# Performance work log

Hardware: AMD Instinct MI355X
Metric: run time of the kernel (lower is better)

Reference implementation:

```python
import jax, jax.numpy as jnp
import numpy as np

NUM_TRAIN = 256  # num_train_anchors
N, A, T = 8, 131072, 64


def _make_boxes(key, shape2):
    # shape2 = (..., 2) of (y, x); returns valid boxes (y1, x1, y2, x2) in [0, 1]
    k1, k2 = jax.random.split(key)
    c1 = jax.random.uniform(k1, shape2, dtype=jnp.float32)
    c2 = jax.random.uniform(k2, shape2, dtype=jnp.float32)
    lo = jnp.minimum(c1, c2)
    hi = jnp.maximum(c1, c2)
    return jnp.stack([lo[..., 0], lo[..., 1], hi[..., 0], hi[..., 1]], axis=-1)


def setup_inputs() -> dict:
    key = jax.random.key(0)
    ka, kt, kp, kn = jax.random.split(key, 4)
    return {
        "anchors": _make_boxes(ka, (N, A, 2)),
        "true_bboxes": _make_boxes(kt, (N, T, 2)),
        "rand_pos": jax.random.uniform(kp, (N, A), dtype=jnp.float32),
        "rand_neg": jax.random.uniform(kn, (N, A), dtype=jnp.float32),
    }


def _bbox_overlap(anchors, gt):
    # anchors [A,4], gt [T,4] -> IoU [A,T]
    ay1, ax1, ay2, ax2 = [anchors[:, i] for i in range(4)]
    gy1, gx1, gy2, gx2 = [gt[:, i] for i in range(4)]
    a_area = (ay2 - ay1) * (ax2 - ax1)                       # [A]
    g_area = (gy2 - gy1) * (gx2 - gx1)                       # [T]
    ih = jnp.clip(jnp.minimum(ay2[:, None], gy2[None, :]) - jnp.maximum(ay1[:, None], gy1[None, :]), 0.0)
    iw = jnp.clip(jnp.minimum(ax2[:, None], gx2[None, :]) - jnp.maximum(ax1[:, None], gx1[None, :]), 0.0)
    inter = ih * iw                                          # [A,T]
    union = a_area[:, None] + g_area[None, :] - inter
    return jnp.where(union > 0, inter / jnp.where(union > 0, union, 1.0), 0.0)


def _rank_of(scores):
    # rank[i] = position of element i in ascending sort of scores
    order = jnp.argsort(scores)
    return jnp.zeros(scores.shape[0], jnp.int32).at[order].set(jnp.arange(scores.shape[0], dtype=jnp.int32))


def _compute_bbox_deltas(anchors, gt):
    # standard (dy, dx, dh, dw) encoding with safe denominators
    ah = anchors[:, 2] - anchors[:, 0]
    aw = anchors[:, 3] - anchors[:, 1]
    acy = anchors[:, 0] + 0.5 * ah
    acx = anchors[:, 1] + 0.5 * aw
    gh = gt[:, 2] - gt[:, 0]
    gw = gt[:, 3] - gt[:, 1]
    gcy = gt[:, 0] + 0.5 * gh
    gcx = gt[:, 1] + 0.5 * gw
    ah_s = jnp.where(ah > 0, ah, 1.0)
    aw_s = jnp.where(aw > 0, aw, 1.0)
    gh_s = jnp.where(gh > 0, gh, 1.0)
    gw_s = jnp.where(gw > 0, gw, 1.0)
    return jnp.stack([(gcy - acy) / ah_s, (gcx - acx) / aw_s,
                      jnp.log(gh_s / ah_s), jnp.log(gw_s / aw_s)], axis=-1)


def _get_targets(anchors, gt, r_pos, r_neg):
    na = anchors.shape[0]
    # strip_out_of_bounds_anchors: zero out anchors falling outside [0,1]^2 (keeps static shape)
    inb = (anchors[:, 0] >= 0) & (anchors[:, 1] >= 0) & (anchors[:, 2] <= 1) & (anchors[:, 3] <= 1)
    anchors = jnp.where(inb[:, None], anchors, 0.0)

    overlaps = _bbox_overlap(anchors, gt)                    # [A,T]

    # --- class assignment ---
    iou_max_val = jnp.max(overlaps, axis=1)                  # [A]
    classes = jnp.full((na,), -1, jnp.int32)
    classes = jnp.where(iou_max_val < 0.3, 0, classes)
    iou_max_anchor = jnp.argmax(overlaps, axis=0)            # [T] best anchor per gt
    pos_anchor = jnp.zeros((na,), jnp.int32).at[iou_max_anchor].set(1)
    classes = jnp.where(pos_anchor > 0, 1, classes)
    classes = jnp.where(iou_max_val >= 0.7, 1, classes)

    # --- subsample positives to NUM_TRAIN//2 (uniform random subset) ---
    pos = classes > 0
    rank_p = _rank_of(jnp.where(pos, r_pos, jnp.inf))
    keep_pos = pos & (rank_p < NUM_TRAIN // 2)
    classes = jnp.where(pos & ~keep_pos, -1, classes)
    n_pos = jnp.sum(keep_pos.astype(jnp.int32))

    # --- subsample negatives to NUM_TRAIN - n_pos ---
    desired_neg = NUM_TRAIN - n_pos
    neg = classes == 0
    rank_n = _rank_of(jnp.where(neg, r_neg, jnp.inf))
    keep_neg = neg & (rank_n < desired_neg)
    classes = jnp.where(neg & ~keep_neg, -1, classes)

    # --- deltas for positive anchors ---
    best_gt = jnp.argmax(overlaps, axis=1)                   # [A]
    deltas = _compute_bbox_deltas(anchors, gt[best_gt])      # [A,4]
    deltas = jnp.where((classes > 0)[:, None], deltas, 0.0)
    return classes, deltas


def reference(anchors, true_bboxes, rand_pos, rand_neg):
    classes, deltas = jax.vmap(_get_targets)(anchors, true_bboxes, rand_pos, rand_neg)
    return classes, deltas
```

## Files before the change

kernel.cpp:

```cpp
#include <hip/hip_runtime.h>
#include <stdint.h>

#define N_B 8
#define A_N 131072
#define T_N 64
#define NUM_TRAIN 256
#define NEG_TAU 0.05f
#define ITEM_CAP 512
#define HSET 512
#define APT 2
#define SEG_A 512
#define GBLK_A 256
#define CAPP 128
#define BLK_C 128
#define SEG_C 1024

typedef unsigned long long u64;
typedef unsigned int u32;

__device__ __forceinline__ u64 aload64(const u64* p) {
    return __hip_atomic_load((u64*)p, __ATOMIC_RELAXED, __HIP_MEMORY_SCOPE_AGENT);
}
__device__ __forceinline__ int aload32(const int* p) {
    return __hip_atomic_load((int*)p, __ATOMIC_RELAXED, __HIP_MEMORY_SCOPE_AGENT);
}
__device__ __forceinline__ void astore64(u64* p, u64 v) {
    __hip_atomic_store(p, v, __ATOMIC_RELAXED, __HIP_MEMORY_SCOPE_AGENT);
}
__device__ __forceinline__ void astore32(int* p, int v) {
    __hip_atomic_store(p, v, __ATOMIC_RELAXED, __HIP_MEMORY_SCOPE_AGENT);
}

__device__ __forceinline__ float iou_one(float ay1, float ax1, float ay2, float ax2,
                                         float a_area, float gy1, float gx1, float gy2,
                                         float gx2, float g_area) {
#pragma clang fp contract(off)
    float ih = fmaxf(fminf(ay2, gy2) - fmaxf(ay1, gy1), 0.0f);
    float iw = fmaxf(fminf(ax2, gx2) - fmaxf(ax1, gx1), 0.0f);
    float inter = ih * iw;
    float uni = (a_area + g_area) - inter;
    return uni > 0.0f ? inter / uni : 0.0f;
}

__device__ __forceinline__ bool in_hset(const int* hset, int a) {
    u32 h = ((u32)a * 2654435761u) >> 23 & (HSET - 1);
    while (true) {
        int v = hset[h];
        if (v == -1) return false;
        if (v == a) return true;
        h = (h + 1) & (HSET - 1);
    }
}

__device__ u64 tail_select(const u64* list, const int* cnts,
                           const u64* extras, int ecnt, const int* hset, bool use_excl,
                           int k, float scale, u64 ovf_all,
                           int* hist, u64* items, int* misc, int* wsum, u64* result) {
    int tid = threadIdx.x, lane = tid & 63, wid = tid >> 6;
    if (tid == 0) { misc[0] = 0; *result = ovf_all; }
    __syncthreads();

    int h = hist[tid], v = h;
#pragma unroll
    for (int d = 1; d < 64; d <<= 1) {
        int t = __shfl_up(v, d, 64);
        if (lane >= d) v += t;
    }
    if (lane == 63) wsum[wid] = v;
    __syncthreads();
    int total = wsum[0] + wsum[1] + wsum[2] + wsum[3];
    int base = 0;
    for (int w = 0; w < wid; w++) base += wsum[w];
    int incl = base + v, exc = incl - h;
    if (k >= exc && k < incl) { misc[1] = tid; misc[2] = exc; }
    if (tid == 0) misc[3] = total;
    __syncthreads();
    if (k >= total) return ovf_all;
    int b = misc[1], before = misc[2];

#define PROC(P) do { u64 p_ = (P); int a_ = (int)(u32)p_;                                   \
        if (!use_excl || !in_hset(hset, a_)) {                                              \
            float v_ = __uint_as_float((u32)(p_ >> 32));                                    \
            int bn_ = (int)(v_ * scale); bn_ = bn_ > 255 ? 255 : bn_;                       \
            if (bn_ == b) { int ix_ = atomicAdd(&misc[0], 1);                               \
                            if (ix_ < ITEM_CAP) items[ix_] = p_; } } } while (0)

    int c = aload32(&cnts[tid]);
    const u64* lp = list + ((size_t)tid << 7);
    for (int ci = 0; ci < c; ci += 4) {
        u64 p0 = aload64(&lp[ci]);
        u64 p1 = (ci + 1 < c) ? aload64(&lp[ci + 1]) : 0;
        u64 p2 = (ci + 2 < c) ? aload64(&lp[ci + 2]) : 0;
        u64 p3 = (ci + 3 < c) ? aload64(&lp[ci + 3]) : 0;
        PROC(p0);
        if (ci + 1 < c) PROC(p1);
        if (ci + 2 < c) PROC(p2);
        if (ci + 3 < c) PROC(p3);
    }
    for (int i = tid; i < ecnt; i += 256) PROC(extras[i]);
#undef PROC
    __syncthreads();
    int m = misc[0]; m = m < ITEM_CAP ? m : ITEM_CAP;
    int target = k - before;
    for (int i = tid; i < m; i += 256) {
        u64 p = items[i];
        int r = 0;
        for (int j = 0; j < m; j++) r += (items[j] < p);
        if (r == target) *result = p;
    }
    __syncthreads();
    u64 res = *result;
    __syncthreads();
    return res;
}

__global__ void __launch_bounds__(256) k_main(const float4* __restrict__ anchors4,
                                              const float4* __restrict__ gts4,
                                              const float* __restrict__ rpos,
                                              const float* __restrict__ rneg,
                                              unsigned char* __restrict__ preclass,
                                              long long* __restrict__ colpack,
                                              u64* __restrict__ pos_list,
                                              u64* __restrict__ neg_list,
                                              int* __restrict__ bcp, int* __restrict__ bcn,
                                              int* __restrict__ hist_pos,
                                              int* __restrict__ hist_neg,
                                              int* __restrict__ done_cnt,
                                              u64* __restrict__ cutoff) {
    __shared__ float4 gbox[T_N];
    __shared__ float gars[T_N];
    __shared__ u64 cmax[T_N];
    __shared__ int lcnt[2];
    __shared__ signed char c0s[SEG_A];
    __shared__ int hist[256];
    __shared__ u64 items[ITEM_CAP];
    __shared__ int hset[HSET];
    __shared__ u64 extras[T_N];
    __shared__ int wnrs[T_N];
    __shared__ int misc[4];
    __shared__ int wsum[4];
    __shared__ int shr[4];
    __shared__ u64 result;
    __shared__ int slast;

    int n = blockIdx.y, bx = blockIdx.x, tid = threadIdx.x, lane = tid & 63;
    int a0 = bx * SEG_A + tid;
    size_t nA = (size_t)n * A_N;

    if (tid < T_N) {
        float4 gb = gts4[n * T_N + tid];
        gbox[tid] = gb;
        {
#pragma clang fp contract(off)
            gars[tid] = (gb.z - gb.x) * (gb.w - gb.y);
        }
        cmax[tid] = 0;
    }
    if (tid < 2) lcnt[tid] = 0;
    __syncthreads();

    float ay1[APT], ax1[APT], ay2[APT], ax2[APT], aar[APT], vmax[APT];
#pragma unroll
    for (int k = 0; k < APT; k++) {
        float4 ab = anchors4[nA + a0 + k * 256];
        float y1 = ab.x, x1 = ab.y, y2 = ab.z, x2 = ab.w;
        bool inb = (y1 >= 0.f) && (x1 >= 0.f) && (y2 <= 1.f) && (x2 <= 1.f);
        if (!inb) { y1 = x1 = y2 = x2 = 0.f; }
        ay1[k] = y1; ax1[k] = x1; ay2[k] = y2; ax2[k] = x2;
        {
#pragma clang fp contract(off)
            aar[k] = (y2 - y1) * (x2 - x1);
        }
        vmax[k] = 0.f;
    }

#pragma unroll 4
    for (int jj = 0; jj < T_N; jj++) {
        int j = (lane + jj) & (T_N - 1);
        float4 gb = gbox[j];
        float gar = gars[j];
        float vb = iou_one(ay1[0], ax1[0], ay2[0], ax2[0], aar[0], gb.x, gb.y, gb.z, gb.w, gar);
        vmax[0] = fmaxf(vmax[0], vb);
        int kb = 0;
#pragma unroll
        for (int k = 1; k < APT; k++) {
            float v = iou_one(ay1[k], ax1[k], ay2[k], ax2[k], aar[k], gb.x, gb.y, gb.z, gb.w, gar);
            vmax[k] = fmaxf(vmax[k], v);
            if (v > vb) { vb = v; kb = k; }
        }
        u64 pk = ((u64)__float_as_uint(vb) << 32) | (u32)(~(u32)(a0 + (kb << 8)));
        atomicMax(&cmax[j], pk);
    }

    size_t segbase = ((size_t)(n * GBLK_A + bx)) << 7;
#pragma unroll
    for (int k = 0; k < APT; k++) {
        int a = a0 + k * 256;
        float vm = vmax[k];
        int c0 = (vm < 0.3f) ? 0 : ((vm >= 0.7f) ? 1 : -1);
        c0s[tid + k * 256] = (signed char)c0;
        preclass[nA + a] = (unsigned char)(signed char)c0;
        if (c0 == 1) {
            float rp = rpos[nA + a];
            int sl = atomicAdd(&lcnt[0], 1);
            if (sl < CAPP) {
                astore64(&pos_list[segbase + sl], ((u64)__float_as_uint(rp) << 32) | (u32)a);
                int bb = (int)(rp * 256.0f); bb = bb > 255 ? 255 : bb;
                atomicAdd(&hist_pos[(n << 8) + bb], 1);
            }
        } else if (c0 == 0) {
            float rn = rneg[nA + a];
            if (rn < NEG_TAU) {
                int sl = atomicAdd(&lcnt[1], 1);
                if (sl < CAPP) {
                    astore64(&neg_list[segbase + sl], ((u64)__float_as_uint(rn) << 32) | (u32)a);
                    int bb = (int)(rn * (256.0f / NEG_TAU)); bb = bb > 255 ? 255 : bb;
                    atomicAdd(&hist_neg[(n << 8) + bb], 1);
                }
            }
        }
    }
    __syncthreads();

    if (tid < T_N) {
        u64 m = cmax[tid];
        u32 wg = ~(u32)m;
        int wl = (int)wg - bx * SEG_A;
        u32 enc = (u32)c0s[wl] & 3u;
        u64 pk = (m & 0xFFFFFFFF00000000ull) | (u32)(~((wg << 2) | enc));
        atomicMax(&colpack[(n << 6) + tid], (long long)pk);
    }
    if (tid == 0) {
        astore32(&bcp[n * GBLK_A + bx], lcnt[0] < CAPP ? lcnt[0] : CAPP);
        astore32(&bcn[n * GBLK_A + bx], lcnt[1] < CAPP ? lcnt[1] : CAPP);
    }

    asm volatile("s_waitcnt vmcnt(0) lgkmcnt(0)" ::: "memory");
    __syncthreads();
    if (tid == 0) slast = (atomicAdd(&done_cnt[n], 1) == GBLK_A - 1) ? 1 : 0;
    __syncthreads();
    if (!slast) return;

    for (int i = tid; i < HSET; i += 256) hset[i] = -1;
    hist[tid] = aload32(&hist_pos[(n << 8) + tid]);
    __syncthreads();

    int w = 0, pcv = 0;
    bool dup = false;
    if (tid < T_N) {
        u64 m = aload64((const u64*)&colpack[(n << 6) + tid]);
        u32 ie = ~(u32)m;
        w = (int)(ie >> 2);
        pcv = ((ie & 3u) == 3u) ? -1 : (int)(ie & 3u);
        wnrs[tid] = w;
        u32 hh = ((u32)w * 2654435761u) >> 23 & (HSET - 1);
        while (true) {
            int old = atomicCAS(&hset[hh], -1, w);
            if (old == -1 || old == w) break;
            hh = (hh + 1) & (HSET - 1);
        }
    }
    __syncthreads();
    if (tid < T_N) {
        for (int t2 = 0; t2 < tid; t2++) dup |= (wnrs[t2] == w);
        bool val = !dup && (pcv != 1);
        u64 mask = __ballot(val);
        if (val) {
            int ix = (int)__popcll(mask & ((1ull << tid) - 1));
            extras[ix] = ((u64)__float_as_uint(rpos[nA + w]) << 32) | (u32)w;
        }
        if (tid == 0) shr[0] = (int)__popcll(mask);
    }
    __syncthreads();
    int extra_cnt = shr[0];
    for (int i = tid; i < extra_cnt; i += 256) {
        float vv = __uint_as_float((u32)(extras[i] >> 32));
        int bb = (int)(vv * 256.0f); bb = bb > 255 ? 255 : bb;
        atomicAdd(&hist[bb], 1);
    }
    __syncthreads();

    u64 cp = tail_select(pos_list + (((size_t)n * GBLK_A) << 7), bcp + n * GBLK_A,
                         extras, extra_cnt, hset, false,
                         NUM_TRAIN / 2, 256.0f, ~0ull,
                         hist, items, misc, wsum, &result);
    int P = misc[3];

    hist[tid] = aload32(&hist_neg[(n << 8) + tid]);
    __syncthreads();
    if (tid < T_N && !dup && pcv == 0) {
        float r = rneg[nA + w];
        if (r < NEG_TAU) {
            int bb = (int)(r * (256.0f / NEG_TAU)); bb = bb > 255 ? 255 : bb;
            atomicAdd(&hist[bb], -1);
        }
    }
    __syncthreads();
    int n_pos = P < NUM_TRAIN / 2 ? P : NUM_TRAIN / 2;
    u64 cn = tail_select(neg_list + (((size_t)n * GBLK_A) << 7), bcn + n * GBLK_A,
                         nullptr, 0, hset, true,
                         NUM_TRAIN - n_pos, 256.0f / NEG_TAU,
                         ((u64)__float_as_uint(NEG_TAU) << 32),
                         hist, items, misc, wsum, &result);
    if (tid == 0) {
        cutoff[2 * n] = cp;
        cutoff[2 * n + 1] = cn;
    }
}

__global__ void __launch_bounds__(256) k_C(const float4* __restrict__ anchors4,
                                           const float4* __restrict__ gts4,
                                           const u32* __restrict__ preclass32,
                                           const long long* __restrict__ colpack,
                                           const float4* __restrict__ rpos4,
                                           const float4* __restrict__ rneg4,
                                           const u64* __restrict__ cutoff,
                                           float4* __restrict__ out_classes4,
                                           float4* __restrict__ out_deltas) {
    __shared__ float4 gbox[T_N];
    __shared__ float gars[T_N];
    __shared__ u32 wbm[32];
    __shared__ u32 pbm[32];
    int n = blockIdx.y, bx = blockIdx.x, tid = threadIdx.x;
    size_t nA = (size_t)n * A_N;
    if (tid < 32) { wbm[tid] = 0; pbm[tid] = 0; }
    __syncthreads();
    if (tid < T_N) {
        float4 gb = gts4[n * T_N + tid];
        gbox[tid] = gb;
        {
#pragma clang fp contract(off)
            gars[tid] = (gb.z - gb.x) * (gb.w - gb.y);
        }
        int w = (int)((~(u32)(u64)colpack[(n << 6) + tid]) >> 2);
        int d = w - bx * SEG_C;
        if ((u32)d < (u32)SEG_C) atomicOr(&wbm[d >> 5], 1u << (d & 31));
    }
    __syncthreads();

    size_t gi4 = nA / 4 + bx * 256 + tid;
    u32 pcw = preclass32[gi4];
    float4 rp = rpos4[gi4];
    float4 rn = rneg4[gi4];
    float rpv[4] = {rp.x, rp.y, rp.z, rp.w};
    float rnv[4] = {rn.x, rn.y, rn.z, rn.w};
    int a0 = (bx * 256 + tid) * 4;
    u64 cp = cutoff[2 * n], cn = cutoff[2 * n + 1];

    u32 marked = (wbm[tid >> 3] >> ((tid & 7) * 4)) & 0xF;

    float fcv[4];
#pragma unroll
    for (int j = 0; j < 4; j++) {
        int c = (int)(signed char)((pcw >> (8 * j)) & 0xFF);
        if ((marked >> j) & 1) c = 1;
        int a = a0 + j;
        int fc = -1;
        if (c == 1) {
            u64 p = ((u64)__float_as_uint(rpv[j]) << 32) | (u32)a;
            fc = (p < cp) ? 1 : -1;
        } else if (c == 0) {
            u64 p = ((u64)__float_as_uint(rnv[j]) << 32) | (u32)a;
            fc = (p < cn) ? 0 : -1;
        }
        fcv[j] = (float)fc;
        if (fc == 1) {
            int s = 4 * tid + j;
            atomicOr(&pbm[s >> 5], 1u << (s & 31));
        }
    }
    out_classes4[gi4] = make_float4(fcv[0], fcv[1], fcv[2], fcv[3]);
    __syncthreads();

    int base = bx * SEG_C;
#pragma unroll
    for (int j = 0; j < 4; j++) {
        int s = j * 256 + tid;
        float4 d = make_float4(0.f, 0.f, 0.f, 0.f);
        if ((pbm[s >> 5] >> (s & 31)) & 1) {
            int a = base + s;
            float4 ab = anchors4[nA + a];
            float ay1 = ab.x, ax1 = ab.y, ay2 = ab.z, ax2 = ab.w;
            bool inb = (ay1 >= 0.f) && (ax1 >= 0.f) && (ay2 <= 1.f) && (ax2 <= 1.f);
            if (!inb) { ay1 = ax1 = ay2 = ax2 = 0.f; }
            float a_area;
            {
#pragma clang fp contract(off)
                a_area = (ay2 - ay1) * (ax2 - ax1);
            }
            float vm = 0.f; int jb = 0;
            for (int t = 0; t < T_N; t++) {
                float4 gb = gbox[t];
                float v = iou_one(ay1, ax1, ay2, ax2, a_area, gb.x, gb.y, gb.z, gb.w, gars[t]);
                bool g = v > vm;
                vm = g ? v : vm;
                jb = g ? t : jb;
            }
            float4 gb = gbox[jb];
            float ah = ay2 - ay1, aw = ax2 - ax1;
            float acy = ay1 + 0.5f * ah, acx = ax1 + 0.5f * aw;
            float gh = gb.z - gb.x, gw = gb.w - gb.y;
            float gcy = gb.x + 0.5f * gh, gcx = gb.y + 0.5f * gw;
            float ah_s = ah > 0.f ? ah : 1.f, aw_s = aw > 0.f ? aw : 1.f;
            float gh_s = gh > 0.f ? gh : 1.f, gw_s = gw > 0.f ? gw : 1.f;
            d.x = (gcy - acy) / ah_s;
            d.y = (gcx - acx) / aw_s;
            d.z = logf(gh_s / ah_s);
            d.w = logf(gw_s / aw_s);
        }
        out_deltas[nA + base + s] = d;
    }
}

extern "C" void kernel_launch(void* const* d_in, const int* in_sizes, int n_in,
                              void* d_out, int out_size, void* d_ws, size_t ws_size,
                              hipStream_t stream) {
    const float4* anchors4 = (const float4*)d_in[0];
    const float4* gts4     = (const float4*)d_in[1];
    const float*  rpos     = (const float*)d_in[2];
    const float*  rneg     = (const float*)d_in[3];

    char* p = (char*)d_ws;
    int* hist_pos_g = (int*)p; p += N_B * 256 * sizeof(int);
    int* hist_neg_g = (int*)p; p += N_B * 256 * sizeof(int);
    int* done_cnt   = (int*)p; p += N_B * sizeof(int);
    u64* cutoff   = (u64*)p;  p += 2 * N_B * sizeof(u64);
    long long* colpack = (long long*)p; p += N_B * T_N * sizeof(long long);
    u64* pos_list = (u64*)p;  p += (size_t)N_B * GBLK_A * CAPP * sizeof(u64);
    u64* neg_list = (u64*)p;  p += (size_t)N_B * GBLK_A * CAPP * sizeof(u64);
    unsigned char* preclass = (unsigned char*)p; p += (size_t)N_B * A_N;
    int* bcp  = (int*)p;  p += N_B * GBLK_A * sizeof(int);
    int* bcn  = (int*)p;  p += N_B * GBLK_A * sizeof(int);

    float4* out_classes4 = (float4*)d_out;
    float4* out_deltas   = (float4*)((float*)d_out + (size_t)N_B * A_N);

    hipMemsetAsync(hist_pos_g, 0, (2 * N_B * 256 + N_B) * sizeof(int), stream);

    k_main<<<dim3(GBLK_A, N_B), 256, 0, stream>>>(anchors4, gts4, rpos, rneg, preclass,
                                                  colpack, pos_list, neg_list, bcp, bcn,
                                                  hist_pos_g, hist_neg_g, done_cnt, cutoff);
    k_C<<<dim3(BLK_C, N_B), 256, 0, stream>>>(anchors4, gts4, (const u32*)preclass,
                                              colpack, (const float4*)rpos,
                                              (const float4*)rneg, cutoff,
                                              out_classes4, out_deltas);
}
```

Measured before the change: 184.7 us.

## Bucket candidate anchors by histogram bin instead of per-block lists

Candidate positive and negative anchors are now written into per-bin global buckets, with slots taken from the histogram atomic counter itself, instead of per-block lists. In the last block's tail selection, only the bucket of the selected bin is scanned rather than every block's list. This removes the per-block shared counters and count arrays and shrinks the serial scan each tail thread does. The cost is heavy global atomic contention on the histogram counters. Candidates are silently dropped if a bin overflows its cap, and the smaller item cap raises the same risk.

Measured after the change: 167.5 us, median of 2. 9.3% less time.

```diff
diff --git a/kernel.cpp b/kernel.cpp
--- a/kernel.cpp
+++ b/kernel.cpp
@@ -6,12 +6,12 @@
 #define T_N 64
 #define NUM_TRAIN 256
 #define NEG_TAU 0.05f
-#define ITEM_CAP 512
+#define ITEM_CAP 256
 #define HSET 512
 #define APT 2
 #define SEG_A 512
 #define GBLK_A 256
-#define CAPP 128
+#define BINCAP 128
 #define BLK_C 128
 #define SEG_C 1024
 
@@ -25,9 +25,6 @@
     return __hip_atomic_load((int*)p, __ATOMIC_RELAXED, __HIP_MEMORY_SCOPE_AGENT);
 }
 __device__ __forceinline__ void astore64(u64* p, u64 v) {
-    __hip_atomic_store(p, v, __ATOMIC_RELAXED, __HIP_MEMORY_SCOPE_AGENT);
-}
-__device__ __forceinline__ void astore32(int* p, int v) {
     __hip_atomic_store(p, v, __ATOMIC_RELAXED, __HIP_MEMORY_SCOPE_AGENT);
 }
 
@@ -52,7 +49,7 @@
     }
 }
 
-__device__ u64 tail_select(const u64* list, const int* cnts,
+__device__ u64 tail_select(const u64* bybin, const int* gcnt,
                            const u64* extras, int ecnt, const int* hset, bool use_excl,
                            int k, float scale, u64 ovf_all,
                            int* hist, u64* items, int* misc, int* wsum, u64* result) {
@@ -78,27 +75,21 @@
     if (k >= total) return ovf_all;
     int b = misc[1], before = misc[2];
 
-#define PROC(P) do { u64 p_ = (P); int a_ = (int)(u32)p_;                                   \
-        if (!use_excl || !in_hset(hset, a_)) {                                              \
-            float v_ = __uint_as_float((u32)(p_ >> 32));                                    \
-            int bn_ = (int)(v_ * scale); bn_ = bn_ > 255 ? 255 : bn_;                       \
-            if (bn_ == b) { int ix_ = atomicAdd(&misc[0], 1);                               \
-                            if (ix_ < ITEM_CAP) items[ix_] = p_; } } } while (0)
-
-    int c = aload32(&cnts[tid]);
-    const u64* lp = list + ((size_t)tid << 7);
-    for (int ci = 0; ci < c; ci += 4) {
-        u64 p0 = aload64(&lp[ci]);
-        u64 p1 = (ci + 1 < c) ? aload64(&lp[ci + 1]) : 0;
-        u64 p2 = (ci + 2 < c) ? aload64(&lp[ci + 2]) : 0;
-        u64 p3 = (ci + 3 < c) ? aload64(&lp[ci + 3]) : 0;
-        PROC(p0);
-        if (ci + 1 < c) PROC(p1);
-        if (ci + 2 < c) PROC(p2);
-        if (ci + 3 < c) PROC(p3);
-    }
-    for (int i = tid; i < ecnt; i += 256) PROC(extras[i]);
-#undef PROC
+    int stored = gcnt[b]; stored = stored > BINCAP ? BINCAP : stored;
+    for (int i = tid; i < stored; i += 256) {
+        u64 p = aload64(&bybin[(size_t)b * BINCAP + i]);
+        int a = (int)(u32)p;
+        if (!use_excl || !in_hset(hset, a)) {
+            int ix = atomicAdd(&misc[0], 1);
+            if (ix < ITEM_CAP) items[ix] = p;
+        }
+    }
+    for (int i = tid; i < ecnt; i += 256) {
+        u64 p = extras[i];
+        float vv = __uint_as_float((u32)(p >> 32));
+        int bn = (int)(vv * scale); bn = bn > 255 ? 255 : bn;
+        if (bn == b) { int ix = atomicAdd(&misc[0], 1); if (ix < ITEM_CAP) items[ix] = p; }
+    }
     __syncthreads();
     int m = misc[0]; m = m < ITEM_CAP ? m : ITEM_CAP;
     int target = k - before;
@@ -120,9 +111,8 @@
                                               const float* __restrict__ rneg,
                                               unsigned char* __restrict__ preclass,
                                               long long* __restrict__ colpack,
-                                              u64* __restrict__ pos_list,
-                                              u64* __restrict__ neg_list,
-                                              int* __restrict__ bcp, int* __restrict__ bcn,
+                                              u64* __restrict__ pos_bybin,
+                                              u64* __restrict__ neg_bybin,
                                               int* __restrict__ hist_pos,
                                               int* __restrict__ hist_neg,
                                               int* __restrict__ done_cnt,
@@ -130,9 +120,9 @@
     __shared__ float4 gbox[T_N];
     __shared__ float gars[T_N];
     __shared__ u64 cmax[T_N];
-    __shared__ int lcnt[2];
     __shared__ signed char c0s[SEG_A];
     __shared__ int hist[256];
+    __shared__ int gcnt[256];
     __shared__ u64 items[ITEM_CAP];
     __shared__ int hset[HSET];
     __shared__ u64 extras[T_N];
@@ -156,7 +146,6 @@
         }
         cmax[tid] = 0;
     }
-    if (tid < 2) lcnt[tid] = 0;
     __syncthreads();
 
     float ay1[APT], ax1[APT], ay2[APT], ax2[APT], aar[APT], vmax[APT];
@@ -192,7 +181,6 @@
         atomicMax(&cmax[j], pk);
     }
 
-    size_t segbase = ((size_t)(n * GBLK_A + bx)) << 7;
 #pragma unroll
     for (int k = 0; k < APT; k++) {
         int a = a0 + k * 256;
@@ -202,21 +190,19 @@
         preclass[nA + a] = (unsigned char)(signed char)c0;
         if (c0 == 1) {
             float rp = rpos[nA + a];
-            int sl = atomicAdd(&lcnt[0], 1);
-            if (sl < CAPP) {
-                astore64(&pos_list[segbase + sl], ((u64)__float_as_uint(rp) << 32) | (u32)a);
-                int bb = (int)(rp * 256.0f); bb = bb > 255 ? 255 : bb;
-                atomicAdd(&hist_pos[(n << 8) + bb], 1);
-            }
+            int bb = (int)(rp * 256.0f); bb = bb > 255 ? 255 : bb;
+            int sl = atomicAdd(&hist_pos[(n << 8) + bb], 1);
+            if (sl < BINCAP)
+                astore64(&pos_bybin[(size_t)((n << 8) + bb) * BINCAP + sl],
+                         ((u64)__float_as_uint(rp) << 32) | (u32)a);
         } else if (c0 == 0) {
             float rn = rneg[nA + a];
             if (rn < NEG_TAU) {
-                int sl = atomicAdd(&lcnt[1], 1);
-                if (sl < CAPP) {
-                    astore64(&neg_list[segbase + sl], ((u64)__float_as_uint(rn) << 32) | (u32)a);
-                    int bb = (int)(rn * (256.0f / NEG_TAU)); bb = bb > 255 ? 255 : bb;
-                    atomicAdd(&hist_neg[(n << 8) + bb], 1);
-                }
+                int bb = (int)(rn * (256.0f / NEG_TAU)); bb = bb > 255 ? 255 : bb;
+                int sl = atomicAdd(&hist_neg[(n << 8) + bb], 1);
+                if (sl < BINCAP)
+                    astore64(&neg_bybin[(size_t)((n << 8) + bb) * BINCAP + sl],
+                             ((u64)__float_as_uint(rn) << 32) | (u32)a);
             }
         }
     }
@@ -230,10 +216,6 @@
         u64 pk = (m & 0xFFFFFFFF00000000ull) | (u32)(~((wg << 2) | enc));
         atomicMax(&colpack[(n << 6) + tid], (long long)pk);
     }
-    if (tid == 0) {
-        astore32(&bcp[n * GBLK_A + bx], lcnt[0] < CAPP ? lcnt[0] : CAPP);
-        astore32(&bcn[n * GBLK_A + bx], lcnt[1] < CAPP ? lcnt[1] : CAPP);
-    }
 
     asm volatile("s_waitcnt vmcnt(0) lgkmcnt(0)" ::: "memory");
     __syncthreads();
@@ -242,7 +224,11 @@
     if (!slast) return;
 
     for (int i = tid; i < HSET; i += 256) hset[i] = -1;
-    hist[tid] = aload32(&hist_pos[(n << 8) + tid]);
+    {
+        int g = aload32(&hist_pos[(n << 8) + tid]);
+        gcnt[tid] = g;
+        hist[tid] = g;
+    }
     __syncthreads();
 
     int w = 0, pcv = 0;
@@ -280,13 +266,17 @@
     }
     __syncthreads();
 
-    u64 cp = tail_select(pos_list + (((size_t)n * GBLK_A) << 7), bcp + n * GBLK_A,
+    u64 cp = tail_select(pos_bybin + ((size_t)(n << 8)) * BINCAP, gcnt,
                          extras, extra_cnt, hset, false,
                          NUM_TRAIN / 2, 256.0f, ~0ull,
                          hist, items, misc, wsum, &result);
     int P = misc[3];
 
-    hist[tid] = aload32(&hist_neg[(n << 8) + tid]);
+    {
+        int g = aload32(&hist_neg[(n << 8) + tid]);
+        gcnt[tid] = g;
+        hist[tid] = g;
+    }
     __syncthreads();
     if (tid < T_N && !dup && pcv == 0) {
         float r = rneg[nA + w];
@@ -297,7 +287,7 @@
     }
     __syncthreads();
     int n_pos = P < NUM_TRAIN / 2 ? P : NUM_TRAIN / 2;
-    u64 cn = tail_select(neg_list + (((size_t)n * GBLK_A) << 7), bcn + n * GBLK_A,
+    u64 cn = tail_select(neg_bybin + ((size_t)(n << 8)) * BINCAP, gcnt,
                          nullptr, 0, hset, true,
                          NUM_TRAIN - n_pos, 256.0f / NEG_TAU,
                          ((u64)__float_as_uint(NEG_TAU) << 32),
@@ -426,11 +416,9 @@
     int* done_cnt   = (int*)p; p += N_B * sizeof(int);
     u64* cutoff   = (u64*)p;  p += 2 * N_B * sizeof(u64);
     long long* colpack = (long long*)p; p += N_B * T_N * sizeof(long long);
-    u64* pos_list = (u64*)p;  p += (size_t)N_B * GBLK_A * CAPP * sizeof(u64);
-    u64* neg_list = (u64*)p;  p += (size_t)N_B * GBLK_A * CAPP * sizeof(u64);
+    u64* pos_bybin = (u64*)p; p += (size_t)N_B * 256 * BINCAP * sizeof(u64);
+    u64* neg_bybin = (u64*)p; p += (size_t)N_B * 256 * BINCAP * sizeof(u64);
     unsigned char* preclass = (unsigned char*)p; p += (size_t)N_B * A_N;
-    int* bcp  = (int*)p;  p += N_B * GBLK_A * sizeof(int);
-    int* bcn  = (int*)p;  p += N_B * GBLK_A * sizeof(int);
 
     float4* out_classes4 = (float4*)d_out;
     float4* out_deltas   = (float4*)((float*)d_out + (size_t)N_B * A_N);
@@ -438,7 +426,7 @@
     hipMemsetAsync(hist_pos_g, 0, (2 * N_B * 256 + N_B) * sizeof(int), stream);
 
     k_main<<<dim3(GBLK_A, N_B), 256, 0, stream>>>(anchors4, gts4, rpos, rneg, preclass,
-                                                  colpack, pos_list, neg_list, bcp, bcn,
+                                                  colpack, pos_bybin, neg_bybin,
                                                   hist_pos_g, hist_neg_g, done_cnt, cutoff);
     k_C<<<dim3(BLK_C, N_B), 256, 0, stream>>>(anchors4, gts4, (const u32*)preclass,
                                               colpack, (const float4*)rpos,
```
